# Optimization experiments

Measured on AMD Instinct MI355X. Metric: run time of the kernel, lower is better.

The kernel has to match this reference:

```python
import jax, jax.numpy as jnp
import numpy as np

N, D, V = 4096, 2048, 50257
IGNORE_INDEX = -100


def setup_inputs() -> dict:
    key = jax.random.key(0)
    k1, k2, k3 = jax.random.split(key, 3)
    x = jax.random.normal(k1, (N, D), dtype=jnp.float32)
    # lm_head.weight is [V, D]; the fused op receives weight.T -> [D, V]
    weight = jax.random.normal(k2, (D, V), dtype=jnp.float32) * (1.0 / np.sqrt(D))
    target = jax.random.randint(k3, (N,), 0, V, dtype=jnp.int64)
    return {"x": x, "weight": weight, "target": target}


def reference(x, weight, target):
    # Fused linear + cross-entropy (reduction='sum'), matching the Helion kernel math:
    # logits accumulated in fp32, online logsumexp == plain stable logsumexp.
    logits = jnp.matmul(x, weight, preferred_element_type=jnp.float32)  # [N, V] fp32
    lse = jax.nn.logsumexp(logits, axis=-1)                              # [N]
    tgt_idx = jnp.clip(target, 0, V - 1)                                 # safe gather
    target_logits = jnp.take_along_axis(logits, tgt_idx[:, None], axis=-1)[:, 0]
    per_token_loss = lse - target_logits                                 # [N]
    mask = (target != IGNORE_INDEX).astype(per_token_loss.dtype)
    ce_loss = jnp.sum(per_token_loss * mask)                             # reduction='sum'
    return ce_loss
```

## Files before the change

kernel.cpp:

```cpp
#include <hip/hip_runtime.h>
#include <hip/hip_bf16.h>
#include <stdint.h>

#define N_TOK 4096
#define DDIM  2048
#define VOCAB 50257
#define IGNORE_INDEX (-100)

#define BM 128
#define BN 128
#define BK 64
#define NT (DDIM / BK)
#define VCHUNKS ((VOCAB + BN - 1) / BN)
#define VP (VCHUNKS * BN)
#define ROW_TILES (N_TOK / BM)
#define GRID_MAIN (VCHUNKS * ROW_TILES)

#define W_SCALE 32.0f
#define W_INV   0.03125f

typedef float f32x4 __attribute__((ext_vector_type(4)));
typedef long  lx2  __attribute__((ext_vector_type(2)));

__device__ __forceinline__ uint32_t pack2bf(float a, float b) {
  uint32_t ua = __float_as_uint(a);
  uint32_t ub = __float_as_uint(b);
  uint32_t ra = (ua + 0x7fffu + ((ua >> 16) & 1u)) >> 16;
  uint32_t rb = (ub + 0x7fffu + ((ub >> 16) & 1u)) & 0xffff0000u;
  return (ra & 0xffffu) | rb;
}

__device__ __forceinline__ uint32_t f32_to_e4m3(float f) {
  uint32_t u = __float_as_uint(f);
  uint32_t s = (u >> 24) & 0x80u;
  float a = fabsf(f);
  if (a >= 448.f) return s | 0x7Eu;
  if (a >= 0.015625f) {
    uint32_t m = __float_as_uint(a);
    m += 0x7FFFFu + ((m >> 20) & 1u);
    uint32_t e = (m >> 23) - 120u;
    return s | (e << 3) | ((m >> 20) & 7u);
  }
  uint32_t m = (uint32_t)rintf(a * 512.f);
  return s | m;
}

__device__ __forceinline__ void gload_lds16(const void* g, void* l) {
  __builtin_amdgcn_global_load_lds(
      (const __attribute__((address_space(1))) uint32_t*)g,
      (__attribute__((address_space(3))) uint32_t*)l, 16, 0, 0);
}


__global__ __launch_bounds__(256) void convert_x8(const float* __restrict__ x,
                                                  uint8_t* __restrict__ x8) {
  int t = blockIdx.x * 256 + threadIdx.x;
  const float4* xp = (const float4*)x + (size_t)t * 4;
  uint32_t u[4];
  #pragma unroll
  for (int g = 0; g < 4; ++g) {
    float4 f = xp[g];
    u[g] = f32_to_e4m3(f.x) | (f32_to_e4m3(f.y) << 8) |
           (f32_to_e4m3(f.z) << 16) | (f32_to_e4m3(f.w) << 24);
  }
  const size_t k0 = (size_t)t * 16;
  uint8_t* out = x8 + ((k0 >> 6) << 6);
  const int h = (int)((k0 >> 5) & 1);
  const int a = (int)((k0 >> 3) & 3);
  *(uint64_t*)(out + a * 16 + h * 8) = (uint64_t)u[0] | ((uint64_t)u[1] << 32);
  *(uint64_t*)(out + (a + 1) * 16 + h * 8) = (uint64_t)u[2] | ((uint64_t)u[3] << 32);
}

__global__ __launch_bounds__(256) void transpose_w8(const float* __restrict__ w,
                                                    uint8_t* __restrict__ w8) {
  __shared__ float t[64][65];
  const int vb = blockIdx.x * 64;
  const int kb = blockIdx.y * 64;
  const int tid = threadIdx.x;
  const int tv = tid & 63, tk4 = tid >> 6;
  #pragma unroll
  for (int i = 0; i < 16; ++i) {
    int kl = tk4 + i * 4;
    int v = vb + tv;
    t[kl][tv] = (v < VOCAB) ? w[(size_t)(kb + kl) * VOCAB + v] * W_SCALE : 0.f;
  }
  __syncthreads();
  const int vl = tid >> 2, seg = tid & 3;
  uint32_t u[4];
  #pragma unroll
  for (int g = 0; g < 4; ++g) {
    const int base = (g < 2) ? (seg * 8 + g * 4) : (32 + seg * 8 + (g - 2) * 4);
    u[g] = 0;
    #pragma unroll
    for (int j = 0; j < 4; ++j)
      u[g] |= f32_to_e4m3(t[base + j][vl]) << (8 * j);
  }
  *(uint4*)(w8 + (size_t)(vb + vl) * DDIM + kb + seg * 16) =
      make_uint4(u[0], u[1], u[2], u[3]);
}

__global__ __launch_bounds__(256, 4) void lmhead_main(
    const uint8_t* __restrict__ w8, const uint8_t* __restrict__ x8,
    const int* __restrict__ tgt,
    float2* __restrict__ partial, float* __restrict__ tlogit)
{
  __shared__ char lds[32768];
  __shared__ float2 stats[2][BM];

  const int bid = blockIdx.x;
  const int v = bid >> 5;
  const int r = bid & 31;
  const int v0 = v * BN;
  const int m0 = r * BM;
  const int tid = threadIdx.x;
  const int lane = tid & 63;
  const int wid = tid >> 6;
  const int wn = wid >> 1, wm = wid & 1;
  const int lr = lane & 15, lk = lane >> 4;

  f32x4 acc[4][4];
  #pragma unroll
  for (int i = 0; i < 4; ++i)
    #pragma unroll
    for (int j = 0; j < 4; ++j) acc[i][j] = (f32x4)0.f;

  const int jj = lane >> 3;
  const int lu_s = (lane & 7) ^ jj;
  const int srow = 2 * jj + (lu_s >> 2);
  const int sk = (lu_s & 3) * 16;
  const uint8_t* wsrc = w8 + (size_t)(v0 + srow) * DDIM + sk;
  const uint8_t* xsrc = x8 + (size_t)(m0 + srow) * DDIM + sk;

  const int jlow = lr >> 1;
  const int lu_r = ((lr & 1) << 2) | lk;
  const int puoff = (lu_r ^ jlow) << 4;
  const int aoff0 = wn * 4096 + jlow * 128 + puoff;
  const int boff0 = wm * 4096 + jlow * 128 + puoff;

  auto stage = [&](int T) {
    char* Al = lds + (T & 1) * 16384;
    char* Bl = Al + 8192;
    const size_t ko = (size_t)T * BK;
    #pragma unroll
    for (int i = 0; i < 2; ++i) {
      int c = wid * 2 + i;
      gload_lds16(wsrc + (size_t)c * 16 * DDIM + ko, Al + c * 1024);
      gload_lds16(xsrc + (size_t)c * 16 * DDIM + ko, Bl + c * 1024);
    }
  };

  stage(0);
  __syncthreads();

  for (int t = 0; t < NT; ++t) {
    if (t + 1 < NT) stage(t + 1);
    const char* Al = lds + (t & 1) * 16384;
    const char* Bl = Al + 8192;
    lx2 av[4], bv[4];
    #pragma unroll
    for (int bi = 0; bi < 4; ++bi)
      av[bi] = *(const lx2*)(Al + aoff0 + bi * 1024);
    #pragma unroll
    for (int bj = 0; bj < 4; ++bj)
      bv[bj] = *(const lx2*)(Bl + boff0 + bj * 1024);
    #pragma unroll
    for (int bi = 0; bi < 4; ++bi)
      #pragma unroll
      for (int bj = 0; bj < 4; ++bj) {
        acc[bi][bj] = __builtin_amdgcn_mfma_f32_16x16x32_fp8_fp8(
            av[bi][0], bv[bj][0], acc[bi][bj], 0, 0, 0);
        acc[bi][bj] = __builtin_amdgcn_mfma_f32_16x16x32_fp8_fp8(
            av[bi][1], bv[bj][1], acc[bi][bj], 0, 0, 0);
      }
    __syncthreads();
  }

  #pragma unroll
  for (int bj = 0; bj < 4; ++bj) {
    const int m_g = m0 + wm * 64 + bj * 16 + lr;
    float vmax = -INFINITY;
    #pragma unroll
    for (int bi = 0; bi < 4; ++bi) {
      #pragma unroll
      for (int rg = 0; rg < 4; ++rg) {
        int n_g = v0 + wn * 64 + bi * 16 + lk * 4 + rg;
        if (n_g < VOCAB) vmax = fmaxf(vmax, acc[bi][bj][rg] * W_INV);
      }
    }
    vmax = fmaxf(vmax, __shfl_xor(vmax, 16, 64));
    vmax = fmaxf(vmax, __shfl_xor(vmax, 32, 64));
    float ssum = 0.f;
    const int t = tgt[m_g];
    #pragma unroll
    for (int bi = 0; bi < 4; ++bi) {
      #pragma unroll
      for (int rg = 0; rg < 4; ++rg) {
        int n_g = v0 + wn * 64 + bi * 16 + lk * 4 + rg;
        float val = acc[bi][bj][rg] * W_INV;
        if (n_g < VOCAB) ssum += __expf(val - vmax);
        if (n_g == t) tlogit[m_g] = val;
      }
    }
    ssum += __shfl_xor(ssum, 16, 64);
    ssum += __shfl_xor(ssum, 32, 64);
    if (lk == 0) stats[wn][wm * 64 + bj * 16 + lr] = make_float2(vmax, ssum);
  }
  __syncthreads();
  if (tid < BM) {
    float2 a = stats[0][tid], b = stats[1][tid];
    float M = fmaxf(a.x, b.x);
    float S = a.y * __expf(a.x - M) + b.y * __expf(b.x - M);
    partial[(size_t)(m0 + tid) * VCHUNKS + v] = make_float2(M, S);
  }
}

typedef short bf16x8 __attribute__((ext_vector_type(8)));

__global__ __launch_bounds__(256, 2) void lmhead_partial_fb(
    const float* __restrict__ x, const float* __restrict__ w,
    const int* __restrict__ tgt,
    float2* __restrict__ partial, float* __restrict__ tlogit)
{
  __shared__ uint4 xs[BM * 64 * 2 / 16];
  __shared__ uint4 wtl[BN * 64 * 2 / 16];
  __shared__ float2 stats[2][BM];

  const int bid = blockIdx.x;
  const int v = bid >> 5;
  const int r = bid & 31;
  const int v0 = v * BN;
  const int m0 = r * BM;
  const int tid = threadIdx.x;
  const int lane = tid & 63;
  const int wid = tid >> 6;
  const int wn = wid >> 1, wm = wid & 1;
  const int lr = lane & 15, lk = lane >> 4;

  f32x4 acc[4][4];
  #pragma unroll
  for (int i = 0; i < 4; ++i)
    #pragma unroll
    for (int j = 0; j < 4; ++j) acc[i][j] = (f32x4)0.f;

  char* xsb = (char*)xs;
  char* wtb = (char*)wtl;

  for (int kt = 0; kt < DDIM / 64; ++kt) {
    const int k0 = kt * 64;
    __syncthreads();
    #pragma unroll
    for (int i = 0; i < 4; ++i) {
      int t = tid + i * 256;
      int m = t >> 3, kg = t & 7;
      const float* gp = x + (size_t)(m0 + m) * DDIM + k0 + kg * 8;
      float4 f0 = *(const float4*)gp;
      float4 f1 = *(const float4*)(gp + 4);
      uint4 pk;
      pk.x = pack2bf(f0.x, f0.y); pk.y = pack2bf(f0.z, f0.w);
      pk.z = pack2bf(f1.x, f1.y); pk.w = pack2bf(f1.z, f1.w);
      int byte = (m * 128 + kg * 16) ^ ((m & 7) << 4);
      *(uint4*)(xsb + byte) = pk;
    }
    #pragma unroll
    for (int i = 0; i < 4; ++i) {
      int t = tid + i * 256;
      int n = t & 127, kg = t >> 7;
      int col = v0 + n;
      float f[8];
      if (col < VOCAB) {
        const float* gp = w + (size_t)(k0 + kg * 8) * VOCAB + col;
        #pragma unroll
        for (int kk = 0; kk < 8; ++kk) f[kk] = gp[(size_t)kk * VOCAB];
      } else {
        #pragma unroll
        for (int kk = 0; kk < 8; ++kk) f[kk] = 0.f;
      }
      uint4 pk;
      pk.x = pack2bf(f[0], f[1]); pk.y = pack2bf(f[2], f[3]);
      pk.z = pack2bf(f[4], f[5]); pk.w = pack2bf(f[6], f[7]);
      int byte = (n * 128 + kg * 16) ^ ((n & 7) << 4);
      *(uint4*)(wtb + byte) = pk;
    }
    __syncthreads();
    #pragma unroll
    for (int ks = 0; ks < 2; ++ks) {
      bf16x8 af[4], bfr[4];
      #pragma unroll
      for (int bi = 0; bi < 4; ++bi) {
        int row = wn * 64 + bi * 16 + lr;
        int byte = (row * 128 + ks * 64 + lk * 16) ^ ((row & 7) << 4);
        af[bi] = *(const bf16x8*)(wtb + byte);
      }
      #pragma unroll
      for (int bj = 0; bj < 4; ++bj) {
        int row = wm * 64 + bj * 16 + lr;
        int byte = (row * 128 + ks * 64 + lk * 16) ^ ((row & 7) << 4);
        bfr[bj] = *(const bf16x8*)(xsb + byte);
      }
      #pragma unroll
      for (int bi = 0; bi < 4; ++bi)
        #pragma unroll
        for (int bj = 0; bj < 4; ++bj)
          acc[bi][bj] = __builtin_amdgcn_mfma_f32_16x16x32_bf16(
              af[bi], bfr[bj], acc[bi][bj], 0, 0, 0);
    }
  }

  #pragma unroll
  for (int bj = 0; bj < 4; ++bj) {
    const int m_g = m0 + wm * 64 + bj * 16 + lr;
    float vmax = -INFINITY;
    #pragma unroll
    for (int bi = 0; bi < 4; ++bi)
      #pragma unroll
      for (int rg = 0; rg < 4; ++rg) {
        int n_g = v0 + wn * 64 + bi * 16 + lk * 4 + rg;
        if (n_g < VOCAB) vmax = fmaxf(vmax, acc[bi][bj][rg]);
      }
    vmax = fmaxf(vmax, __shfl_xor(vmax, 16, 64));
    vmax = fmaxf(vmax, __shfl_xor(vmax, 32, 64));
    float ssum = 0.f;
    const int t = tgt[m_g];
    #pragma unroll
    for (int bi = 0; bi < 4; ++bi)
      #pragma unroll
      for (int rg = 0; rg < 4; ++rg) {
        int n_g = v0 + wn * 64 + bi * 16 + lk * 4 + rg;
        float val = acc[bi][bj][rg];
        if (n_g < VOCAB) ssum += __expf(val - vmax);
        if (n_g == t) tlogit[m_g] = val;
      }
    ssum += __shfl_xor(ssum, 16, 64);
    ssum += __shfl_xor(ssum, 32, 64);
    if (lk == 0) stats[wn][wm * 64 + bj * 16 + lr] = make_float2(vmax, ssum);
  }
  __syncthreads();
  if (tid < BM) {
    float2 a = stats[0][tid], b = stats[1][tid];
    float M = fmaxf(a.x, b.x);
    float S = a.y * __expf(a.x - M) + b.y * __expf(b.x - M);
    partial[(size_t)(m0 + tid) * VCHUNKS + v] = make_float2(M, S);
  }
}

__device__ __forceinline__ void lse_merge(float& m, float& s, float M, float S) {
  if (S > 0.f) {
    if (M > m) { s = s * __expf(m - M) + S; m = M; }
    else       { s += S * __expf(M - m); }
  }
}

__global__ void lmhead_reduce(const float2* __restrict__ partial,
                              const float* __restrict__ tlogit,
                              const int* __restrict__ tgt,
                              float* __restrict__ out)
{
  const int wid = threadIdx.x >> 6;
  const int lane = threadIdx.x & 63;
  const int row = blockIdx.x * 4 + wid;
  float m = -INFINITY, s = 0.f;
  for (int c = lane; c < VCHUNKS; c += 64) {
    float2 p = partial[(size_t)row * VCHUNKS + c];
    lse_merge(m, s, p.x, p.y);
  }
  #pragma unroll
  for (int off = 1; off < 64; off <<= 1) {
    float M = __shfl_xor(m, off, 64);
    float S = __shfl_xor(s, off, 64);
    lse_merge(m, s, M, S);
  }
  if (lane == 0) {
    int t = tgt[row];
    if (t != IGNORE_INDEX) {
      float loss = m + __logf(s) - tlogit[row];
      atomicAdd(out, loss);
    }
  }
}

extern "C" void kernel_launch(void* const* d_in, const int* in_sizes, int n_in,
                              void* d_out, int out_size, void* d_ws, size_t ws_size,
                              hipStream_t stream) {
  const float* x = (const float*)d_in[0];
  const float* w = (const float*)d_in[1];
  const int* tgt = (const int*)d_in[2];
  float* out = (float*)d_out;

  const size_t w8_bytes = (size_t)VP * DDIM;
  const size_t x8_bytes = (size_t)N_TOK * DDIM;
  const size_t part_bytes = (size_t)N_TOK * VCHUNKS * 8;
  const size_t tl_bytes = (size_t)N_TOK * 4;
  const size_t need = w8_bytes + x8_bytes + part_bytes + tl_bytes;

  hipMemsetAsync(d_out, 0, sizeof(float), stream);

  if (ws_size >= need) {
    uint8_t* w8 = (uint8_t*)d_ws;
    uint8_t* x8 = (uint8_t*)d_ws + w8_bytes;
    float2* partial = (float2*)((char*)d_ws + w8_bytes + x8_bytes);
    float* tlogit = (float*)((char*)d_ws + w8_bytes + x8_bytes + part_bytes);

    convert_x8<<<dim3(N_TOK * DDIM / 16 / 256), 256, 0, stream>>>(x, x8);
    transpose_w8<<<dim3(VP / 64, DDIM / 64), 256, 0, stream>>>(w, w8);
    lmhead_main<<<dim3(GRID_MAIN), 256, 0, stream>>>(w8, x8, tgt, partial, tlogit);
    lmhead_reduce<<<dim3(N_TOK / 4), 256, 0, stream>>>(partial, tlogit, tgt, out);
  } else {
    float2* partial = (float2*)d_ws;
    float* tlogit = (float*)((char*)d_ws + part_bytes);
    lmhead_partial_fb<<<dim3(GRID_MAIN), 256, 0, stream>>>(x, w, tgt, partial, tlogit);
    lmhead_reduce<<<dim3(N_TOK / 4), 256, 0, stream>>>(partial, tlogit, tgt, out);
  }
}
```

Before: 770.4 us.

## Switch FP8 GEMM to 32x32x64 scaled MFMA with matching LDS layout

Replaces the 16x16x32 fp8 MFMA tiles with the MI355 gfx950 32x32x64 f8f6f4 scaled MFMA using unit scales. The fp8 packing in the x and w conversion kernels, the swizzled LDS read offsets and the epilogue row/column mapping are all changed to fit the new operand and accumulator layout. This halves the MFMA instruction count per K-tile and uses the higher-throughput instruction. In exchange it changes LDS access patterns, which risks bank conflicts and layout mistakes.

After: 747.2 us. -3.0%, faster.

```diff
diff --git a/kernel.cpp b/kernel.cpp
--- a/kernel.cpp
+++ b/kernel.cpp
@@ -18,9 +18,12 @@
 
 #define W_SCALE 32.0f
 #define W_INV   0.03125f
-
-typedef float f32x4 __attribute__((ext_vector_type(4)));
-typedef long  lx2  __attribute__((ext_vector_type(2)));
+#define SCALE_1 0x7F7F7F7FU
+
+typedef float f32x4  __attribute__((ext_vector_type(4)));
+typedef float f32x16 __attribute__((ext_vector_type(16)));
+typedef int   i32x4  __attribute__((ext_vector_type(4)));
+typedef int   i32x8  __attribute__((ext_vector_type(8)));
 
 __device__ __forceinline__ uint32_t pack2bf(float a, float b) {
   uint32_t ua = __float_as_uint(a);
@@ -51,7 +54,6 @@
       (__attribute__((address_space(3))) uint32_t*)l, 16, 0, 0);
 }
 
-
 __global__ __launch_bounds__(256) void convert_x8(const float* __restrict__ x,
                                                   uint8_t* __restrict__ x8) {
   int t = blockIdx.x * 256 + threadIdx.x;
@@ -63,12 +65,7 @@
     u[g] = f32_to_e4m3(f.x) | (f32_to_e4m3(f.y) << 8) |
            (f32_to_e4m3(f.z) << 16) | (f32_to_e4m3(f.w) << 24);
   }
-  const size_t k0 = (size_t)t * 16;
-  uint8_t* out = x8 + ((k0 >> 6) << 6);
-  const int h = (int)((k0 >> 5) & 1);
-  const int a = (int)((k0 >> 3) & 3);
-  *(uint64_t*)(out + a * 16 + h * 8) = (uint64_t)u[0] | ((uint64_t)u[1] << 32);
-  *(uint64_t*)(out + (a + 1) * 16 + h * 8) = (uint64_t)u[2] | ((uint64_t)u[3] << 32);
+  ((uint4*)x8)[t] = make_uint4(u[0], u[1], u[2], u[3]);
 }
 
 __global__ __launch_bounds__(256) void transpose_w8(const float* __restrict__ w,
@@ -89,11 +86,10 @@
   uint32_t u[4];
   #pragma unroll
   for (int g = 0; g < 4; ++g) {
-    const int base = (g < 2) ? (seg * 8 + g * 4) : (32 + seg * 8 + (g - 2) * 4);
     u[g] = 0;
     #pragma unroll
     for (int j = 0; j < 4; ++j)
-      u[g] |= f32_to_e4m3(t[base + j][vl]) << (8 * j);
+      u[g] |= f32_to_e4m3(t[seg * 16 + g * 4 + j][vl]) << (8 * j);
   }
   *(uint4*)(w8 + (size_t)(vb + vl) * DDIM + kb + seg * 16) =
       make_uint4(u[0], u[1], u[2], u[3]);
@@ -116,13 +112,12 @@
   const int lane = tid & 63;
   const int wid = tid >> 6;
   const int wn = wid >> 1, wm = wid & 1;
-  const int lr = lane & 15, lk = lane >> 4;
-
-  f32x4 acc[4][4];
-  #pragma unroll
-  for (int i = 0; i < 4; ++i)
-    #pragma unroll
-    for (int j = 0; j < 4; ++j) acc[i][j] = (f32x4)0.f;
+
+  f32x16 acc[2][2];
+  #pragma unroll
+  for (int i = 0; i < 2; ++i)
+    #pragma unroll
+    for (int j = 0; j < 2; ++j) acc[i][j] = (f32x16)0.f;
 
   const int jj = lane >> 3;
   const int lu_s = (lane & 7) ^ jj;
@@ -131,11 +126,12 @@
   const uint8_t* wsrc = w8 + (size_t)(v0 + srow) * DDIM + sk;
   const uint8_t* xsrc = x8 + (size_t)(m0 + srow) * DDIM + sk;
 
-  const int jlow = lr >> 1;
-  const int lu_r = ((lr & 1) << 2) | lk;
-  const int puoff = (lu_r ^ jlow) << 4;
-  const int aoff0 = wn * 4096 + jlow * 128 + puoff;
-  const int boff0 = wm * 4096 + jlow * 128 + puoff;
+  const int r5 = lane & 31, hi = lane >> 5;
+  const int j7 = (r5 >> 1) & 7;
+  const int lu0 = ((r5 & 1) << 2) | (hi << 1);
+  const int rdoff = (r5 >> 1) * 128 + ((lu0 ^ j7) << 4);
+  const int aoff0 = wn * 32 * 128 + rdoff;
+  const int boff0 = wm * 32 * 128 + rdoff;
 
   auto stage = [&](int T) {
     char* Al = lds + (T & 1) * 16384;
@@ -156,54 +152,56 @@
     if (t + 1 < NT) stage(t + 1);
     const char* Al = lds + (t & 1) * 16384;
     const char* Bl = Al + 8192;
-    lx2 av[4], bv[4];
-    #pragma unroll
-    for (int bi = 0; bi < 4; ++bi)
-      av[bi] = *(const lx2*)(Al + aoff0 + bi * 1024);
-    #pragma unroll
-    for (int bj = 0; bj < 4; ++bj)
-      bv[bj] = *(const lx2*)(Bl + boff0 + bj * 1024);
-    #pragma unroll
-    for (int bi = 0; bi < 4; ++bi)
-      #pragma unroll
-      for (int bj = 0; bj < 4; ++bj) {
-        acc[bi][bj] = __builtin_amdgcn_mfma_f32_16x16x32_fp8_fp8(
-            av[bi][0], bv[bj][0], acc[bi][bj], 0, 0, 0);
-        acc[bi][bj] = __builtin_amdgcn_mfma_f32_16x16x32_fp8_fp8(
-            av[bi][1], bv[bj][1], acc[bi][bj], 0, 0, 0);
-      }
+    i32x8 av[2], bv[2];
+    #pragma unroll
+    for (int bi = 0; bi < 2; ++bi) {
+      i32x4 a0 = *(const i32x4*)(Al + aoff0 + bi * 2048);
+      i32x4 a1 = *(const i32x4*)(Al + (aoff0 ^ 16) + bi * 2048);
+      av[bi] = __builtin_shufflevector(a0, a1, 0, 1, 2, 3, 4, 5, 6, 7);
+    }
+    #pragma unroll
+    for (int bj = 0; bj < 2; ++bj) {
+      i32x4 b0 = *(const i32x4*)(Bl + boff0 + bj * 2048);
+      i32x4 b1 = *(const i32x4*)(Bl + (boff0 ^ 16) + bj * 2048);
+      bv[bj] = __builtin_shufflevector(b0, b1, 0, 1, 2, 3, 4, 5, 6, 7);
+    }
+    #pragma unroll
+    for (int bi = 0; bi < 2; ++bi)
+      #pragma unroll
+      for (int bj = 0; bj < 2; ++bj)
+        acc[bi][bj] = __builtin_amdgcn_mfma_scale_f32_32x32x64_f8f6f4(
+            av[bi], bv[bj], acc[bi][bj], 0 , 0 ,
+            0, SCALE_1, 0, SCALE_1);
     __syncthreads();
   }
 
   #pragma unroll
-  for (int bj = 0; bj < 4; ++bj) {
-    const int m_g = m0 + wm * 64 + bj * 16 + lr;
+  for (int bj = 0; bj < 2; ++bj) {
+    const int m_g = m0 + wm * 64 + bj * 32 + r5;
     float vmax = -INFINITY;
     #pragma unroll
-    for (int bi = 0; bi < 4; ++bi) {
-      #pragma unroll
-      for (int rg = 0; rg < 4; ++rg) {
-        int n_g = v0 + wn * 64 + bi * 16 + lk * 4 + rg;
+    for (int bi = 0; bi < 2; ++bi) {
+      #pragma unroll
+      for (int rg = 0; rg < 16; ++rg) {
+        int n_g = v0 + wn * 64 + bi * 32 + (rg & 3) + 8 * (rg >> 2) + 4 * hi;
         if (n_g < VOCAB) vmax = fmaxf(vmax, acc[bi][bj][rg] * W_INV);
       }
     }
-    vmax = fmaxf(vmax, __shfl_xor(vmax, 16, 64));
     vmax = fmaxf(vmax, __shfl_xor(vmax, 32, 64));
     float ssum = 0.f;
     const int t = tgt[m_g];
     #pragma unroll
-    for (int bi = 0; bi < 4; ++bi) {
-      #pragma unroll
-      for (int rg = 0; rg < 4; ++rg) {
-        int n_g = v0 + wn * 64 + bi * 16 + lk * 4 + rg;
+    for (int bi = 0; bi < 2; ++bi) {
+      #pragma unroll
+      for (int rg = 0; rg < 16; ++rg) {
+        int n_g = v0 + wn * 64 + bi * 32 + (rg & 3) + 8 * (rg >> 2) + 4 * hi;
         float val = acc[bi][bj][rg] * W_INV;
         if (n_g < VOCAB) ssum += __expf(val - vmax);
         if (n_g == t) tlogit[m_g] = val;
       }
     }
-    ssum += __shfl_xor(ssum, 16, 64);
     ssum += __shfl_xor(ssum, 32, 64);
-    if (lk == 0) stats[wn][wm * 64 + bj * 16 + lr] = make_float2(vmax, ssum);
+    if (hi == 0) stats[wn][wm * 64 + bj * 32 + r5] = make_float2(vmax, ssum);
   }
   __syncthreads();
   if (tid < BM) {
```
